# Kernel optimization log

Hardware: AMD Instinct MI355X
Metric: run time of the kernel (lower is better)

The kernel has to match this reference:

```python
import jax, jax.numpy as jnp
import numpy as np

B, D_IN, D_FEAT, N_EX, N_LAB = 4096, 512, 512, 20000, 100
P_FACTOR = 3.0
EPS = 1e-12  # torch F.normalize eps


def setup_inputs() -> dict:
    key = jax.random.key(0)
    k1, k2, k3, k4 = jax.random.split(key, 4)
    features = jax.random.normal(k1, (B, D_IN), dtype=jnp.float32)
    g_weight = jax.random.normal(k2, (D_FEAT, D_IN), dtype=jnp.float32) * (1.0 / np.sqrt(D_IN))
    ex_features = jax.random.normal(k3, (N_EX, D_IN), dtype=jnp.float32)
    ex_classes = jax.random.uniform(k4, (N_EX, N_LAB), dtype=jnp.float32)
    class_reps = jnp.eye(N_LAB, dtype=jnp.float32)  # one_hot(arange(num_labels)) since class_dim is None
    return {"features": features, "g_weight": g_weight, "ex_features": ex_features,
            "ex_classes": ex_classes, "class_reps": class_reps}


def _l2_normalize(x):
    n = jnp.linalg.norm(x, axis=-1, keepdims=True)
    return x / jnp.maximum(n, EPS)


def _l1_normalize(x):
    n = jnp.sum(jnp.abs(x), axis=-1, keepdims=True)
    return x / jnp.maximum(n, EPS)


def reference(features, g_weight, ex_features, ex_classes, class_reps):
    # g projection (bias-free linear)
    f = features @ g_weight.T          # [B, D_FEAT]
    e = ex_features @ g_weight.T       # [N_EX, D_FEAT]
    # exemplar class representations
    ex_class_reps = _l1_normalize(ex_classes) @ class_reps  # [N_EX, N_LAB]
    # cosine similarity
    s = _l2_normalize(f) @ _l2_normalize(e).T  # [B, N_EX]
    # power-sign activation then L1 row-normalize
    a = jnp.sign(s) * jnp.abs(s) ** P_FACTOR
    a = _l1_normalize(a)
    echo = a @ ex_class_reps           # [B, N_LAB]
    return echo
```

## Files before the change

### kernel.cpp

```cpp
#include <hip/hip_runtime.h>

#define B_ROWS 4096
#define D      512
#define N_EX   20000
#define EXP2   20096
#define MPROJ  24192
#define N_LAB  100
#define LABP2  128
#define NT2    157
#define SPLITS 16

typedef __attribute__((ext_vector_type(8)))  short short8v;
typedef __attribute__((ext_vector_type(4)))  short short4v;
typedef __attribute__((ext_vector_type(16))) float f32x16;
typedef __attribute__((ext_vector_type(2)))  int   int2v;
typedef unsigned short u16;

__device__ __forceinline__ u16 f2bf(float x) {
    unsigned u = __builtin_bit_cast(unsigned, x);
    u = u + 0x7FFFu + ((u >> 16) & 1u);
    return (u16)(u >> 16);
}
__device__ __forceinline__ float bf2f(u16 h) {
    unsigned u = ((unsigned)h) << 16;
    return __builtin_bit_cast(float, u);
}

__device__ __forceinline__ float wave_reduce_sum(float v) {
    #pragma unroll
    for (int off = 32; off > 0; off >>= 1) v += __shfl_down(v, off, 64);
    return v;
}

__device__ __forceinline__ void gload16(const void* g, void* l) {
    __builtin_amdgcn_global_load_lds((const __attribute__((address_space(1))) void*)g,
                                     (__attribute__((address_space(3))) void*)l, 16, 0, 0);
}

__device__ __forceinline__ unsigned pk_bf16(float a, float b) {
    unsigned r;
    asm("v_cvt_pk_bf16_f32 %0, %1, %2" : "=v"(r) : "v"(a), "v"(b));
    return r;
}

__device__ __forceinline__ void swap_halves(unsigned &a, unsigned &b) {
#if __has_builtin(__builtin_amdgcn_permlane32_swap)
    int2v r = __builtin_amdgcn_permlane32_swap((int)a, (int)b, false, false);
    a = (unsigned)r[0]; b = (unsigned)r[1];
#else
    unsigned sa = (unsigned)__shfl_xor((int)a, 32, 64);
    unsigned sb = (unsigned)__shfl_xor((int)b, 32, 64);
    if (threadIdx.x & 32) a = sb; else b = sa;
#endif
}

#define MFMA32(a, b, c) __builtin_amdgcn_mfma_f32_32x32x16_bf16((a), (b), (c), 0, 0, 0)

__global__ __launch_bounds__(256)
void splitH_k(const float* __restrict__ src, u16* __restrict__ dst,
              int src_rows, int dst_rows) {
    int i8 = blockIdx.x * 256 + threadIdx.x;
    if (i8 >= dst_rows * 64) return;
    int row = i8 >> 6;
    int e = (i8 & 63) * 8;
    short8v h = {0,0,0,0,0,0,0,0};
    if (row < src_rows) {
        const float* p = &src[(size_t)row * D + e];
        float4 a = *(const float4*)p, b = *(const float4*)(p + 4);
        float v[8] = {a.x,a.y,a.z,a.w,b.x,b.y,b.z,b.w};
        #pragma unroll
        for (int j = 0; j < 8; ++j) h[j] = (short)f2bf(v[j]);
    }
    *(short8v*)&dst[(size_t)row * D + e] = h;
}

__global__ __launch_bounds__(512, 4)
void gemm128_k(const u16* __restrict__ A, const u16* __restrict__ B,
               u16* __restrict__ C) {
    __shared__ u16 BUF[2][128][128];
    const int tid = threadIdx.x;
    const int l = tid & 63, w = tid >> 6;
    const int wa = w >> 2, wb = w & 3;
    const int l31 = l & 31, l5 = l >> 5;
    const int m0 = blockIdx.x * 128, n0 = blockIdx.y * 128;
    const int qrow_in = l >> 4;
    const int gs = l & 15;

    f32x16 sacc[2] = {};

    auto STAGE = [&](int nx, int kc_) {
        const int kofs = kc_ * 64;
        #pragma unroll
        for (int i = 0; i < 4; ++i) {
            const int q = w * 4 + i;
            const int r = q * 4 + qrow_in;
            const int g = gs ^ (r & 15);
            const u16* src = (g < 8)
                ? &A[(size_t)(m0 + r) * D + kofs + g * 8]
                : &B[(size_t)(n0 + r) * D + kofs + (g - 8) * 8];
            gload16(src, (u16*)&BUF[nx][0][0] + q * 512);
        }
    };

    STAGE(0, 0);
    __syncthreads();
    int cur = 0;
    for (int kc = 0; kc < 8; ++kc) {
        if (kc < 7) STAGE(cur ^ 1, kc + 1);
        const u16* base = &BUF[cur][0][0];
        #pragma unroll
        for (int ks = 0; ks < 4; ++ks) {
            const int gk = ks * 2 + l5;
            short8v aX[2], bW;
            #pragma unroll
            for (int ei = 0; ei < 2; ++ei) {
                int r = wa * 64 + ei * 32 + l31;
                aX[ei] = *(const short8v*)(base + r * 128 + (gk ^ (r & 15)) * 8);
            }
            {
                int r = wb * 32 + l31;
                bW = *(const short8v*)(base + r * 128 + ((gk | 8) ^ (r & 15)) * 8);
            }
            sacc[0] = MFMA32(aX[0], bW, sacc[0]);
            sacc[1] = MFMA32(aX[1], bW, sacc[1]);
        }
        __syncthreads();
        cur ^= 1;
    }
    #pragma unroll
    for (int ei = 0; ei < 2; ++ei)
        #pragma unroll
        for (int r = 0; r < 16; ++r) {
            int row = m0 + wa * 64 + ei * 32 + (r & 3) + 8 * (r >> 2) + 4 * l5;
            int col = n0 + wb * 32 + l31;
            C[(size_t)row * D + col] = f2bf(sacc[ei][r]);
        }
}

__global__ __launch_bounds__(128)
void l2norm_k(u16* __restrict__ hi) {
    const int row = blockIdx.x, tid = threadIdx.x;
    const size_t base = (size_t)row * D + tid * 4;
    short4v hv = *(short4v*)&hi[base];
    float v[4]; float ss = 0.f;
    #pragma unroll
    for (int j = 0; j < 4; ++j) { v[j] = bf2f((u16)hv[j]); ss += v[j] * v[j]; }
    ss = wave_reduce_sum(ss);
    __shared__ float red[2];
    if ((tid & 63) == 0) red[tid >> 6] = ss;
    __syncthreads();
    float inv = 1.0f / fmaxf(sqrtf(red[0] + red[1]), 1e-12f);
    short4v ho;
    #pragma unroll
    for (int j = 0; j < 4; ++j) ho[j] = (short)f2bf(v[j] * inv);
    *(short4v*)&hi[base] = ho;
}

__global__ __launch_bounds__(256)
void ecrT_k(const float* __restrict__ exc, const float* __restrict__ creps,
            u16* __restrict__ th) {
    __shared__ float CRT[N_LAB][101];
    __shared__ float EX[128][N_LAB];
    __shared__ float INV[128];
    __shared__ u16 OUT[LABP2][128];
    const int tid = threadIdx.x;
    const int e0 = blockIdx.x * 128;
    for (int i = tid; i < N_LAB * N_LAB; i += 256) {
        int c = i / N_LAB, lab = i % N_LAB;
        CRT[lab][c] = creps[i];
    }
    for (int i = tid; i < 128 * N_LAB; i += 256) {
        int el = i / N_LAB, c = i % N_LAB;
        int e = e0 + el;
        EX[el][c] = (e < N_EX) ? exc[(size_t)e * N_LAB + c] : 0.f;
    }
    __syncthreads();
    if (tid < 128) {
        float s = 0.f;
        for (int c = 0; c < N_LAB; ++c) s += fabsf(EX[tid][c]);
        INV[tid] = 1.0f / fmaxf(s, 1e-12f);
    }
    __syncthreads();
    const int lab = tid & 127;
    for (int el = tid >> 7; el < 128; el += 2) {
        float acc = 0.f;
        if (lab < N_LAB) {
            #pragma unroll 4
            for (int c = 0; c < N_LAB; ++c) acc += EX[el][c] * CRT[lab][c];
            acc *= INV[el];
        }
        OUT[lab][el] = f2bf(acc);
    }
    __syncthreads();
    for (int i = tid; i < LABP2 * 16; i += 256) {
        int lb = i >> 4, ch = i & 15;
        *(short8v*)&th[(size_t)lb * EXP2 + e0 + ch * 8] = *(const short8v*)&OUT[lb][ch * 8];
    }
}

__global__ __launch_bounds__(512, 2)
void fused_k(const u16* __restrict__ fnh, const u16* __restrict__ enh,
             const u16* __restrict__ ecth,
             float* __restrict__ nump, float* __restrict__ denp2) {
    __shared__ u16 SMEM[65536];
    u16* ENR = SMEM;
    u16* FNR = SMEM + 16384;
    u16* WTB = SMEM + 49152;

    const int tid = threadIdx.x;
    const int l = tid & 63, w = tid >> 6;
    const int we = w >> 2, wq = w & 3;
    const int l31 = l & 31, l5 = l >> 5;
    const int m0 = blockIdx.x * 256;
    const int split = blockIdx.y;

    union FragU { short8v s; unsigned u[4]; };

    f32x16 num_acc[2][4] = {};
    float den_th[2] = {0.f, 0.f};

    auto STAGE_AB = [&](int nx, int t_, int kc_) {
        const int e0_ = t_ * 128, kofs = kc_ * 64;
        #pragma unroll
        for (int i = 0; i < 2; ++i) {
            const int ge = w * 128 + i * 64 + l;
            const int row = ge >> 3, g = ge & 7;
            gload16(&enh[(size_t)(e0_ + row) * D + kofs + ((g ^ (row & 7)) * 8)],
                    ENR + nx * 8192 + (w * 128 + i * 64) * 8);
        }
        #pragma unroll
        for (int i = 0; i < 4; ++i) {
            const int gf = w * 256 + i * 64 + l;
            const int row = gf >> 3, g = gf & 7;
            gload16(&fnh[(size_t)(m0 + row) * D + kofs + ((g ^ (row & 7)) * 8)],
                    FNR + nx * 16384 + (w * 256 + i * 64) * 8);
        }
    };
    auto STAGE_WT = [&](int t_) {
        const int e0_ = t_ * 128;
        #pragma unroll
        for (int i = 0; i < 4; ++i) {
            const int gwt = w * 256 + i * 64 + l;
            const int lab = gwt >> 4, g = gwt & 15;
            gload16(&ecth[(size_t)lab * EXP2 + e0_ + ((g ^ (lab & 15)) * 8)],
                    WTB + (w * 256 + i * 64) * 8);
        }
    };

    STAGE_AB(0, split, 0);
    __syncthreads();
    int cur = 0;

    for (int t = split; t < NT2; t += SPLITS) {
        f32x16 sacc[2][2] = {};
        for (int kc = 0; kc < 8; ++kc) {
            if (kc < 7) STAGE_AB(cur ^ 1, t, kc + 1);
            else        STAGE_WT(t);
            const u16* eb = ENR + cur * 8192;
            const u16* fb = FNR + cur * 16384;
            #pragma unroll
            for (int ks = 0; ks < 4; ++ks) {
                const int gk = ks * 2 + l5;
                short8v aE[2], bF[2];
                #pragma unroll
                for (int ei = 0; ei < 2; ++ei) {
                    int r = we * 64 + ei * 32 + l31;
                    aE[ei] = *(const short8v*)(eb + r * 64 + (gk ^ (r & 7)) * 8);
                }
                #pragma unroll
                for (int mi = 0; mi < 2; ++mi) {
                    int r = wq * 64 + mi * 32 + l31;
                    bF[mi] = *(const short8v*)(fb + r * 64 + (gk ^ (r & 7)) * 8);
                }
                #pragma unroll
                for (int ei = 0; ei < 2; ++ei)
                    #pragma unroll
                    for (int mi = 0; mi < 2; ++mi)
                        sacc[ei][mi] = MFMA32(aE[ei], bF[mi], sacc[ei][mi]);
            }
            __syncthreads();
            if (kc < 7) cur ^= 1;
        }
        const int tn = t + SPLITS;
        if (tn < NT2) STAGE_AB(cur ^ 1, tn, 0);
        #pragma unroll
        for (int ei = 0; ei < 2; ++ei) {
            FragU fr[2][2];
            #pragma unroll
            for (int mi = 0; mi < 2; ++mi) {
                float a3[16];
                #pragma unroll
                for (int r = 0; r < 16; ++r) {
                    float sv = sacc[ei][mi][r];
                    float c3 = sv * sv * sv;
                    a3[r] = c3;
                    den_th[mi] += fabsf(c3);
                }
                #pragma unroll
                for (int c = 0; c < 2; ++c) {
                    unsigned p01 = pk_bf16(a3[c*8+0], a3[c*8+1]);
                    unsigned p23 = pk_bf16(a3[c*8+2], a3[c*8+3]);
                    unsigned p45 = pk_bf16(a3[c*8+4], a3[c*8+5]);
                    unsigned p67 = pk_bf16(a3[c*8+6], a3[c*8+7]);
                    swap_halves(p01, p45);
                    swap_halves(p23, p67);
                    fr[mi][c].u[0] = p01; fr[mi][c].u[1] = p23;
                    fr[mi][c].u[2] = p45; fr[mi][c].u[3] = p67;
                }
            }
            #pragma unroll
            for (int c = 0; c < 2; ++c) {
                const int gw = (we * 4 + ei * 2 + c) * 2 + l5;
                #pragma unroll
                for (int lt = 0; lt < 4; ++lt) {
                    int row = lt * 32 + l31;
                    short8v wf = *(const short8v*)(WTB + row * 128 + (gw ^ (row & 15)) * 8);
                    num_acc[0][lt] = MFMA32(fr[0][c].s, wf, num_acc[0][lt]);
                    num_acc[1][lt] = MFMA32(fr[1][c].s, wf, num_acc[1][lt]);
                }
            }
        }
        __syncthreads();
        cur ^= 1;
    }

    #pragma unroll
    for (int mi = 0; mi < 2; ++mi) {
        float v = den_th[mi];
        v += __shfl_xor(v, 32, 64);
        if (l5 == 0)
            denp2[((size_t)split * 2 + we) * B_ROWS + m0 + wq * 64 + mi * 32 + l31] = v;
    }

    float* SMf = (float*)SMEM;
    __syncthreads();
    #pragma unroll
    for (int half = 0; half < 2; ++half) {
        if (we == 1 && (wq >> 1) == half) {
            #pragma unroll
            for (int mi = 0; mi < 2; ++mi)
                #pragma unroll
                for (int lt = 0; lt < 4; ++lt)
                    #pragma unroll
                    for (int r = 0; r < 16; ++r) {
                        int rowf = (r & 3) + 8 * (r >> 2) + 4 * l5;
                        int lrow = (wq & 1) * 64 + mi * 32 + rowf;
                        SMf[lrow * 128 + lt * 32 + l31] = num_acc[mi][lt][r];
                    }
        }
        __syncthreads();
        if (we == 0 && (wq >> 1) == half) {
            #pragma unroll
            for (int mi = 0; mi < 2; ++mi)
                #pragma unroll
                for (int lt = 0; lt < 4; ++lt)
                    #pragma unroll
                    for (int r = 0; r < 16; ++r) {
                        int rowf = (r & 3) + 8 * (r >> 2) + 4 * l5;
                        int lrow = (wq & 1) * 64 + mi * 32 + rowf;
                        float v = num_acc[mi][lt][r] + SMf[lrow * 128 + lt * 32 + l31];
                        int m = m0 + wq * 64 + mi * 32 + rowf;
                        nump[((size_t)split * B_ROWS + m) * LABP2 + lt * 32 + l31] = v;
                    }
        }
        __syncthreads();
    }
}

__global__ __launch_bounds__(128)
void finalize_k(const float* __restrict__ nump, const float* __restrict__ denp2,
                float* __restrict__ out) {
    const int row = blockIdx.x, tid = threadIdx.x;
    float den = 0.f;
    for (int s = 0; s < 2 * SPLITS; ++s)
        den += denp2[(size_t)s * B_ROWS + row];
    if (tid < N_LAB) {
        float acc = 0.f;
        for (int s = 0; s < SPLITS; ++s)
            acc += nump[((size_t)s * B_ROWS + row) * LABP2 + tid];
        out[(size_t)row * N_LAB + tid] = acc / fmaxf(den, 1e-12f);
    }
}

extern "C" void kernel_launch(void* const* d_in, const int* in_sizes, int n_in,
                              void* d_out, int out_size, void* d_ws, size_t ws_size,
                              hipStream_t stream) {
    (void)in_sizes; (void)n_in; (void)out_size; (void)ws_size;
    const float* features    = (const float*)d_in[0];
    const float* g_weight    = (const float*)d_in[1];
    const float* ex_features = (const float*)d_in[2];
    const float* ex_classes  = (const float*)d_in[3];
    const float* class_reps  = (const float*)d_in[4];
    float* out = (float*)d_out;

    size_t off = 0;
    auto alloc = [&](size_t bytes) {
        void* p = (char*)d_ws + off;
        off += (bytes + 255) & ~(size_t)255;
        return p;
    };
    u16* fnh = (u16*)alloc((size_t)B_ROWS * D * 2);
    u16* enh = (u16*)alloc((size_t)EXP2 * D * 2);
    u16* ecth = (u16*)alloc((size_t)LABP2 * EXP2 * 2);
    u16* wh  = (u16*)alloc((size_t)D * D * 2);
    float* nump  = (float*)alloc((size_t)SPLITS * B_ROWS * LABP2 * 4);
    float* denp2 = (float*)alloc((size_t)2 * SPLITS * B_ROWS * 4);
    u16* xall = (u16*)nump;

    splitH_k<<<(B_ROWS * 64 + 255) / 256, 256, 0, stream>>>(features, xall, B_ROWS, B_ROWS);
    splitH_k<<<(EXP2 * 64 + 255) / 256, 256, 0, stream>>>(ex_features, xall + (size_t)B_ROWS * D, N_EX, EXP2);
    splitH_k<<<(D * 64 + 255) / 256, 256, 0, stream>>>(g_weight, wh, D, D);
    gemm128_k<<<dim3(MPROJ / 128, 4), 512, 0, stream>>>(xall, wh, fnh);
    l2norm_k<<<MPROJ, 128, 0, stream>>>(fnh);
    ecrT_k<<<NT2, 256, 0, stream>>>(ex_classes, class_reps, ecth);
    fused_k<<<dim3(B_ROWS / 256, SPLITS), 512, 0, stream>>>(fnh, enh, ecth, nump, denp2);
    finalize_k<<<B_ROWS, 128, 0, stream>>>(nump, denp2, out);
}
```

Before: 380.7 us.

## Merge conversion launches, wave-per-row l2norm, repack fused LDS tiles, fine-grained waits

The three fp32-to-bf16 conversion launches are merged into one kernel, and l2norm now gives each row to a single wave with 8-element vectors and a shuffle reduction instead of a shared-memory reduction. In the fused kernel, the LDS tiles are repacked so two 64-wide rows share a 128-element line with a 16-way XOR swizzle. The full __syncthreads barriers are replaced with explicit vmcnt/lgkmcnt waits plus s_barrier, so the next tile's global-to-LDS copies can stay in flight during compute. MFMA sections are also wrapped in s_setprio; the hand-counted waits risk races if the in-flight load counts do not match.

Measured after the change: 400.7 us. 1.05x slower.

```diff
diff --git a/kernel.cpp b/kernel.cpp
--- a/kernel.cpp
+++ b/kernel.cpp
@@ -11,7 +11,6 @@
 #define SPLITS 16
 
 typedef __attribute__((ext_vector_type(8)))  short short8v;
-typedef __attribute__((ext_vector_type(4)))  short short4v;
 typedef __attribute__((ext_vector_type(16))) float f32x16;
 typedef __attribute__((ext_vector_type(2)))  int   int2v;
 typedef unsigned short u16;
@@ -24,12 +23,6 @@
 __device__ __forceinline__ float bf2f(u16 h) {
     unsigned u = ((unsigned)h) << 16;
     return __builtin_bit_cast(float, u);
-}
-
-__device__ __forceinline__ float wave_reduce_sum(float v) {
-    #pragma unroll
-    for (int off = 32; off > 0; off >>= 1) v += __shfl_down(v, off, 64);
-    return v;
 }
 
 __device__ __forceinline__ void gload16(const void* g, void* l) {
@@ -57,21 +50,34 @@
 #define MFMA32(a, b, c) __builtin_amdgcn_mfma_f32_32x32x16_bf16((a), (b), (c), 0, 0, 0)
 
 __global__ __launch_bounds__(256)
-void splitH_k(const float* __restrict__ src, u16* __restrict__ dst,
-              int src_rows, int dst_rows) {
+void split3_k(const float* __restrict__ f, const float* __restrict__ ex,
+              const float* __restrict__ gw, u16* __restrict__ xall,
+              u16* __restrict__ wh) {
     int i8 = blockIdx.x * 256 + threadIdx.x;
-    if (i8 >= dst_rows * 64) return;
     int row = i8 >> 6;
     int e = (i8 & 63) * 8;
+    const float* src = nullptr;
+    u16* dst;
+    if (row < B_ROWS) {
+        src = &f[(size_t)row * D + e];
+        dst = &xall[(size_t)row * D + e];
+    } else if (row < B_ROWS + EXP2) {
+        int er = row - B_ROWS;
+        if (er < N_EX) src = &ex[(size_t)er * D + e];
+        dst = &xall[(size_t)row * D + e];
+    } else if (row < B_ROWS + EXP2 + D) {
+        int wr = row - B_ROWS - EXP2;
+        src = &gw[(size_t)wr * D + e];
+        dst = &wh[(size_t)wr * D + e];
+    } else return;
     short8v h = {0,0,0,0,0,0,0,0};
-    if (row < src_rows) {
-        const float* p = &src[(size_t)row * D + e];
-        float4 a = *(const float4*)p, b = *(const float4*)(p + 4);
+    if (src) {
+        float4 a = *(const float4*)src, b = *(const float4*)(src + 4);
         float v[8] = {a.x,a.y,a.z,a.w,b.x,b.y,b.z,b.w};
         #pragma unroll
         for (int j = 0; j < 8; ++j) h[j] = (short)f2bf(v[j]);
     }
-    *(short8v*)&dst[(size_t)row * D + e] = h;
+    *(short8v*)dst = h;
 }
 
 __global__ __launch_bounds__(512, 4)
@@ -137,23 +143,23 @@
         }
 }
 
-__global__ __launch_bounds__(128)
-void l2norm_k(u16* __restrict__ hi) {
-    const int row = blockIdx.x, tid = threadIdx.x;
-    const size_t base = (size_t)row * D + tid * 4;
-    short4v hv = *(short4v*)&hi[base];
-    float v[4]; float ss = 0.f;
-    #pragma unroll
-    for (int j = 0; j < 4; ++j) { v[j] = bf2f((u16)hv[j]); ss += v[j] * v[j]; }
-    ss = wave_reduce_sum(ss);
-    __shared__ float red[2];
-    if ((tid & 63) == 0) red[tid >> 6] = ss;
-    __syncthreads();
-    float inv = 1.0f / fmaxf(sqrtf(red[0] + red[1]), 1e-12f);
-    short4v ho;
-    #pragma unroll
-    for (int j = 0; j < 4; ++j) ho[j] = (short)f2bf(v[j] * inv);
-    *(short4v*)&hi[base] = ho;
+__global__ __launch_bounds__(256)
+void l2norm_k(u16* __restrict__ hi, int nrows) {
+    const int row = blockIdx.x * 4 + (threadIdx.x >> 6);
+    const int ln = threadIdx.x & 63;
+    if (row >= nrows) return;
+    const size_t base = (size_t)row * D + ln * 8;
+    short8v hv = *(short8v*)&hi[base];
+    float v[8]; float ss = 0.f;
+    #pragma unroll
+    for (int j = 0; j < 8; ++j) { v[j] = bf2f((u16)hv[j]); ss += v[j] * v[j]; }
+    #pragma unroll
+    for (int off = 32; off > 0; off >>= 1) ss += __shfl_xor(ss, off, 64);
+    float inv = 1.0f / fmaxf(sqrtf(ss), 1e-12f);
+    short8v ho;
+    #pragma unroll
+    for (int j = 0; j < 8; ++j) ho[j] = (short)f2bf(v[j] * inv);
+    *(short8v*)&hi[base] = ho;
 }
 
 __global__ __launch_bounds__(256)
@@ -223,66 +229,86 @@
         const int e0_ = t_ * 128, kofs = kc_ * 64;
         #pragma unroll
         for (int i = 0; i < 2; ++i) {
-            const int ge = w * 128 + i * 64 + l;
-            const int row = ge >> 3, g = ge & 7;
-            gload16(&enh[(size_t)(e0_ + row) * D + kofs + ((g ^ (row & 7)) * 8)],
-                    ENR + nx * 8192 + (w * 128 + i * 64) * 8);
+            const int p = w * 128 + i * 64 + l;
+            const int line = p >> 4, q = (p & 15) ^ (line & 15);
+            const int row = line * 2 + (q >> 3), g = q & 7;
+            gload16(&enh[(size_t)(e0_ + row) * D + kofs + g * 8],
+                    ENR + nx * 8192 + p * 8);
         }
         #pragma unroll
         for (int i = 0; i < 4; ++i) {
-            const int gf = w * 256 + i * 64 + l;
-            const int row = gf >> 3, g = gf & 7;
-            gload16(&fnh[(size_t)(m0 + row) * D + kofs + ((g ^ (row & 7)) * 8)],
-                    FNR + nx * 16384 + (w * 256 + i * 64) * 8);
+            const int p = w * 256 + i * 64 + l;
+            const int line = p >> 4, q = (p & 15) ^ (line & 15);
+            const int row = line * 2 + (q >> 3), g = q & 7;
+            gload16(&fnh[(size_t)(m0 + row) * D + kofs + g * 8],
+                    FNR + nx * 16384 + p * 8);
         }
     };
     auto STAGE_WT = [&](int t_) {
         const int e0_ = t_ * 128;
         #pragma unroll
         for (int i = 0; i < 4; ++i) {
-            const int gwt = w * 256 + i * 64 + l;
-            const int lab = gwt >> 4, g = gwt & 15;
+            const int p = w * 256 + i * 64 + l;
+            const int lab = p >> 4, g = p & 15;
             gload16(&ecth[(size_t)lab * EXP2 + e0_ + ((g ^ (lab & 15)) * 8)],
-                    WTB + (w * 256 + i * 64) * 8);
+                    WTB + p * 8);
         }
     };
+    auto ldfrag = [&](const u16* base, int r, int gk) -> short8v {
+        int line = r >> 1;
+        int slot = (((r & 1) << 3) | gk) ^ (line & 15);
+        return *(const short8v*)(base + line * 128 + slot * 8);
+    };
 
     STAGE_AB(0, split, 0);
-    __syncthreads();
     int cur = 0;
 
     for (int t = split; t < NT2; t += SPLITS) {
         f32x16 sacc[2][2] = {};
         for (int kc = 0; kc < 8; ++kc) {
-            if (kc < 7) STAGE_AB(cur ^ 1, t, kc + 1);
-            else        STAGE_WT(t);
+            if (kc < 7) {
+                STAGE_AB(cur ^ 1, t, kc + 1);
+                asm volatile("s_waitcnt vmcnt(6)" ::: "memory");
+            } else {
+                STAGE_WT(t);
+                asm volatile("s_waitcnt vmcnt(4)" ::: "memory");
+            }
+            __builtin_amdgcn_s_barrier();
+            __builtin_amdgcn_sched_barrier(0);
             const u16* eb = ENR + cur * 8192;
             const u16* fb = FNR + cur * 16384;
+            __builtin_amdgcn_s_setprio(1);
             #pragma unroll
             for (int ks = 0; ks < 4; ++ks) {
                 const int gk = ks * 2 + l5;
                 short8v aE[2], bF[2];
                 #pragma unroll
-                for (int ei = 0; ei < 2; ++ei) {
-                    int r = we * 64 + ei * 32 + l31;
-                    aE[ei] = *(const short8v*)(eb + r * 64 + (gk ^ (r & 7)) * 8);
-                }
-                #pragma unroll
-                for (int mi = 0; mi < 2; ++mi) {
-                    int r = wq * 64 + mi * 32 + l31;
-                    bF[mi] = *(const short8v*)(fb + r * 64 + (gk ^ (r & 7)) * 8);
-                }
+                for (int ei = 0; ei < 2; ++ei)
+                    aE[ei] = ldfrag(eb, we * 64 + ei * 32 + l31, gk);
+                #pragma unroll
+                for (int mi = 0; mi < 2; ++mi)
+                    bF[mi] = ldfrag(fb, wq * 64 + mi * 32 + l31, gk);
                 #pragma unroll
                 for (int ei = 0; ei < 2; ++ei)
                     #pragma unroll
                     for (int mi = 0; mi < 2; ++mi)
                         sacc[ei][mi] = MFMA32(aE[ei], bF[mi], sacc[ei][mi]);
             }
-            __syncthreads();
+            __builtin_amdgcn_s_setprio(0);
+            asm volatile("s_waitcnt lgkmcnt(0)" ::: "memory");
+            __builtin_amdgcn_sched_barrier(0);
+            __builtin_amdgcn_s_barrier();
             if (kc < 7) cur ^= 1;
         }
         const int tn = t + SPLITS;
-        if (tn < NT2) STAGE_AB(cur ^ 1, tn, 0);
+        if (tn < NT2) {
+            STAGE_AB(cur ^ 1, tn, 0);
+            asm volatile("s_waitcnt vmcnt(6)" ::: "memory");
+        } else {
+            asm volatile("s_waitcnt vmcnt(0)" ::: "memory");
+        }
+        __builtin_amdgcn_s_barrier();
+        __builtin_amdgcn_sched_barrier(0);
         #pragma unroll
         for (int ei = 0; ei < 2; ++ei) {
             FragU fr[2][2];
@@ -308,6 +334,7 @@
                     fr[mi][c].u[2] = p45; fr[mi][c].u[3] = p67;
                 }
             }
+            __builtin_amdgcn_s_setprio(1);
             #pragma unroll
             for (int c = 0; c < 2; ++c) {
                 const int gw = (we * 4 + ei * 2 + c) * 2 + l5;
@@ -319,8 +346,11 @@
                     num_acc[1][lt] = MFMA32(fr[1][c].s, wf, num_acc[1][lt]);
                 }
             }
-        }
-        __syncthreads();
+            __builtin_amdgcn_s_setprio(0);
+        }
+        asm volatile("s_waitcnt lgkmcnt(0)" ::: "memory");
+        __builtin_amdgcn_sched_barrier(0);
+        __builtin_amdgcn_s_barrier();
         cur ^= 1;
     }
 
@@ -407,11 +437,11 @@
     float* denp2 = (float*)alloc((size_t)2 * SPLITS * B_ROWS * 4);
     u16* xall = (u16*)nump;
 
-    splitH_k<<<(B_ROWS * 64 + 255) / 256, 256, 0, stream>>>(features, xall, B_ROWS, B_ROWS);
-    splitH_k<<<(EXP2 * 64 + 255) / 256, 256, 0, stream>>>(ex_features, xall + (size_t)B_ROWS * D, N_EX, EXP2);
-    splitH_k<<<(D * 64 + 255) / 256, 256, 0, stream>>>(g_weight, wh, D, D);
+    const int tot_rows = B_ROWS + EXP2 + D;
+    split3_k<<<(tot_rows * 64 + 255) / 256, 256, 0, stream>>>(
+        features, ex_features, g_weight, xall, wh);
     gemm128_k<<<dim3(MPROJ / 128, 4), 512, 0, stream>>>(xall, wh, fnh);
-    l2norm_k<<<MPROJ, 128, 0, stream>>>(fnh);
+    l2norm_k<<<(MPROJ + 3) / 4, 256, 0, stream>>>(fnh, MPROJ);
     ecrT_k<<<NT2, 256, 0, stream>>>(ex_classes, class_reps, ecth);
     fused_k<<<dim3(B_ROWS / 256, SPLITS), 512, 0, stream>>>(fnh, enh, ecth, nump, denp2);
     finalize_k<<<B_ROWS, 128, 0, stream>>>(nump, denp2, out);
```
